# Performance work log

Hardware: AMD Instinct MI355X
Metric: run time of the kernel (lower is better)

## Reference

```python
import jax, jax.numpy as jnp
import numpy as np

C = 256
NUM_HEADS = 8
GROUPS = 8
EPS = 1e-5


def setup_inputs() -> dict:
    key = jax.random.key(0)
    ks = jax.random.split(key, 7)
    B, H, W = 2, 64, 64
    x = jax.random.normal(ks[0], (B, C, H, W), dtype=jnp.float32)
    gn_weight = jnp.ones((C,), dtype=jnp.float32)
    gn_bias = jnp.zeros((C,), dtype=jnp.float32)
    # 1x1 convs == per-pixel linear layers
    w_qkv = jax.random.normal(ks[1], (3 * C, C), dtype=jnp.float32) * (1.0 / np.sqrt(C))
    b_qkv = jax.random.normal(ks[2], (3 * C,), dtype=jnp.float32) * 0.01
    w_proj = jax.random.normal(ks[3], (C, C), dtype=jnp.float32) * (1.0 / np.sqrt(C))
    b_proj = jax.random.normal(ks[4], (C,), dtype=jnp.float32) * 0.01
    return {"x": x, "gn_weight": gn_weight, "gn_bias": gn_bias,
            "w_qkv": w_qkv, "b_qkv": b_qkv, "w_proj": w_proj, "b_proj": b_proj}


def reference(x, gn_weight, gn_bias, w_qkv, b_qkv, w_proj, b_proj):
    B, Cc, H, W = x.shape
    nh = NUM_HEADS
    hd = Cc // nh
    N = H * W
    scale = hd ** (-0.5)

    # GroupNorm(8, C): normalize over (C/G, H, W) per group, biased variance
    xg = x.reshape(B, GROUPS, Cc // GROUPS, H, W)
    mean = xg.mean(axis=(2, 3, 4), keepdims=True)
    var = xg.var(axis=(2, 3, 4), keepdims=True)
    hn = (xg - mean) * jax.lax.rsqrt(var + EPS)
    hn = hn.reshape(B, Cc, H, W) * gn_weight[None, :, None, None] + gn_bias[None, :, None, None]

    hf = hn.reshape(B, Cc, N)                       # [B, C, N]
    qkv = jnp.einsum('oc,bcn->bon', w_qkv, hf) + b_qkv[None, :, None]  # [B, 3C, N]
    qkv = qkv.reshape(B, 3, nh, hd, N)
    # q,k,v: [B, nh, N, hd]
    q = jnp.transpose(qkv[:, 0], (0, 1, 3, 2))
    k = jnp.transpose(qkv[:, 1], (0, 1, 3, 2))
    v = jnp.transpose(qkv[:, 2], (0, 1, 3, 2))

    attn = jnp.einsum('bhqd,bhkd->bhqk', q, k) * scale  # [B, nh, N, N]
    attn = jax.nn.softmax(attn, axis=-1)
    o = jnp.einsum('bhqk,bhkd->bhqd', attn, v)           # [B, nh, N, hd]
    o = jnp.transpose(o, (0, 1, 3, 2)).reshape(B, Cc, H, W)

    of = o.reshape(B, Cc, N)
    out = jnp.einsum('oc,bcn->bon', w_proj, of) + b_proj[None, :, None]
    return out.reshape(B, Cc, H, W)
```

## Files before the change

kernel.cpp:

```cpp
#include <hip/hip_runtime.h>


typedef _Float16 half8 __attribute__((ext_vector_type(8)));
typedef __fp16   fp16x2 __attribute__((ext_vector_type(2)));
typedef float    f32x4 __attribute__((ext_vector_type(4)));
typedef int      int2v __attribute__((ext_vector_type(2)));
typedef int      int4v __attribute__((ext_vector_type(4)));

__device__ __forceinline__ f32x4 mfma16(half8 a, half8 b, f32x4 c) {
  return __builtin_amdgcn_mfma_f32_16x16x32_f16(a, b, c, 0, 0, 0);
}

#if __has_builtin(__builtin_amdgcn_exp2f)
#define EXP2(x) __builtin_amdgcn_exp2f(x)
#else
#define EXP2(x) exp2f(x)
#endif

__device__ __forceinline__ unsigned short h_bits(_Float16 h) {
  return __builtin_bit_cast(unsigned short, h);
}
__device__ __forceinline__ int h2_bits(fp16x2 h) {
  return __builtin_bit_cast(int, h);
}

constexpr float CSCALE = (float)(1.4426950408889634 / 5.656854249492381);

__global__ __launch_bounds__(256) void gn_stats(const float* __restrict__ x,
                                                float* __restrict__ stats) {
  const int bg = blockIdx.x, ch = blockIdx.y, tid = threadIdx.x;
  const float* p = x + (size_t)bg * 131072 + (size_t)ch * 4096;
  float s = 0.f, ss = 0.f;
#pragma unroll
  for (int j = 0; j < 4; ++j) {
    f32x4 v = *(const f32x4*)(p + j * 1024 + tid * 4);
#pragma unroll
    for (int k = 0; k < 4; ++k) { s += v[k]; ss += v[k] * v[k]; }
  }
#pragma unroll
  for (int m = 1; m <= 32; m <<= 1) { s += __shfl_xor(s, m); ss += __shfl_xor(ss, m); }
  __shared__ float red[8];
  const int wv = tid >> 6;
  if ((tid & 63) == 0) { red[wv * 2] = s; red[wv * 2 + 1] = ss; }
  __syncthreads();
  if (tid == 0) {
    float S = red[0] + red[2] + red[4] + red[6];
    float SS = red[1] + red[3] + red[5] + red[7];
    atomicAdd(&stats[bg * 2], S);
    atomicAdd(&stats[bg * 2 + 1], SS);
  }
}

__global__ __launch_bounds__(256) void gn_apply(const float* __restrict__ x,
                                                const float* __restrict__ gw,
                                                const float* __restrict__ gb,
                                                const float* __restrict__ stats,
                                                _Float16* __restrict__ hn) {
  __shared__ float tile[64 * 65];
  const int tid = threadIdx.x;
  const int a = tid & 15;
  const int row16 = tid >> 4;
  const int b = blockIdx.z, c0 = blockIdx.y * 64, n0 = blockIdx.x * 64;
#pragma unroll
  for (int m = 0; m < 4; ++m) {
    const int cl = row16 + 16 * m;
    const int c = c0 + cl;
    const int g = c >> 5;
    const float s = stats[(b * 8 + g) * 2];
    const float ss = stats[(b * 8 + g) * 2 + 1];
    const float mean = s * (1.f / 131072.f);
    const float var = ss * (1.f / 131072.f) - mean * mean;
    const float rstd = rsqrtf(var + 1e-5f);
    const float ga = gw[c] * rstd;
    const float be = gb[c] - mean * ga;
    f32x4 xv = *(const f32x4*)(x + ((size_t)(b * 256 + c)) * 4096 + n0 + a * 4);
#pragma unroll
    for (int j = 0; j < 4; ++j) tile[cl * 65 + a * 4 + j] = xv[j] * ga + be;
  }
  __syncthreads();
#pragma unroll
  for (int m = 0; m < 4; ++m) {
    const int nl = row16 + 16 * m;
    const int cb = a * 4;
    int2v uh;
    unsigned short hh[4];
#pragma unroll
    for (int j = 0; j < 4; ++j) {
      hh[j] = h_bits((_Float16)tile[(cb + j) * 65 + nl]);
    }
    uh[0] = hh[0] | (hh[1] << 16); uh[1] = hh[2] | (hh[3] << 16);
    size_t off = ((size_t)(b * 4096 + n0 + nl)) * 256 + c0 + cb;
    *(int2v*)(hn + off) = uh;
  }
}

__global__ __launch_bounds__(256) void wcast(const float* __restrict__ wq,
                                             const float* __restrict__ wp,
                                             _Float16* __restrict__ wqh,
                                             _Float16* __restrict__ wph) {
  const int idx = blockIdx.x * 256 + threadIdx.x;
  if (idx < 196608) {
    wqh[idx] = (_Float16)wq[idx];
  } else {
    wph[idx - 196608] = (_Float16)wp[idx - 196608];
  }
}

template <int MODE>
__global__ __launch_bounds__(256) void gemm_f16(
    const _Float16* __restrict__ W, const _Float16* __restrict__ Bm,
    const float* __restrict__ bias,
    _Float16* __restrict__ qkT, _Float16* __restrict__ v_t,
    float* __restrict__ outp) {
  __shared__ _Float16 a_lds[2][4096];
  __shared__ _Float16 b_lds[2][4096];
  const int tid = threadIdx.x, lane = tid & 63, wv = tid >> 6;
  const int qq = lane >> 4, ii = lane & 15;
  const int m0 = blockIdx.x * 64, n0 = blockIdx.y * 64, bz = blockIdx.z;

  const _Float16* asrc[2];
  const _Float16* bsrc[2];
  int dst8[2];
#pragma unroll
  for (int rep = 0; rep < 2; ++rep) {
    const int idx = tid + 256 * rep;
    dst8[rep] = idx * 8;
    const int j = idx >> 7, c = (idx >> 6) & 1, l = idx & 63;
    const int lq = l >> 4, li = l & 15;
    asrc[rep] = W + (size_t)(m0 + 16 * j + li) * 256 + 32 * c + 8 * lq;
    bsrc[rep] = Bm + ((size_t)(bz * 4096 + n0 + 16 * j + li)) * 256 + 32 * c + 8 * lq;
  }

  f32x4 acc[4] = {};

  half8 ar0 = *(const half8*)asrc[0];
  half8 ar1 = *(const half8*)asrc[1];
  half8 br0 = *(const half8*)bsrc[0];
  half8 br1 = *(const half8*)bsrc[1];
  *(half8*)(a_lds[0] + dst8[0]) = ar0;
  *(half8*)(a_lds[0] + dst8[1]) = ar1;
  *(half8*)(b_lds[0] + dst8[0]) = br0;
  *(half8*)(b_lds[0] + dst8[1]) = br1;
  __syncthreads();

  for (int it = 0; it < 4; ++it) {
    const int cur = it & 1;
    if (it < 3) {
      const int ko = (it + 1) * 64;
      ar0 = *(const half8*)(asrc[0] + ko);
      ar1 = *(const half8*)(asrc[1] + ko);
      br0 = *(const half8*)(bsrc[0] + ko);
      br1 = *(const half8*)(bsrc[1] + ko);
    }
    half8 ah0 = *(const half8*)(a_lds[cur] + ((wv * 2 + 0) * 64 + lane) * 8);
    half8 ah1 = *(const half8*)(a_lds[cur] + ((wv * 2 + 1) * 64 + lane) * 8);
#pragma unroll
    for (int t = 0; t < 4; ++t) {
      half8 b0 = *(const half8*)(b_lds[cur] + ((t * 2 + 0) * 64 + lane) * 8);
      half8 b1 = *(const half8*)(b_lds[cur] + ((t * 2 + 1) * 64 + lane) * 8);
      acc[t] = mfma16(ah0, b0, acc[t]);
      acc[t] = mfma16(ah1, b1, acc[t]);
    }
    if (it < 3) {
      _Float16* an = a_lds[cur ^ 1];
      _Float16* bn = b_lds[cur ^ 1];
      *(half8*)(an + dst8[0]) = ar0;
      *(half8*)(an + dst8[1]) = ar1;
      *(half8*)(bn + dst8[0]) = br0;
      *(half8*)(bn + dst8[1]) = br1;
    }
    __syncthreads();
  }

  const int och0 = m0 + 16 * wv + 4 * qq;
  if (MODE == 0) {
    if (m0 < 512) {
      const float sc = (m0 < 256) ? CSCALE : 1.0f;
#pragma unroll
      for (int t = 0; t < 4; ++t) {
        const int n = n0 + 16 * t + ii;
        unsigned short hh[4];
#pragma unroll
        for (int r = 0; r < 4; ++r) {
          hh[r] = h_bits((_Float16)((acc[t][r] + bias[och0 + r]) * sc));
        }
        int2v u;
        u[0] = hh[0] | (hh[1] << 16);
        u[1] = hh[2] | (hh[3] << 16);
        *(int2v*)(qkT + ((size_t)(bz * 4096 + n)) * 512 + och0) = u;
      }
    } else {
#pragma unroll
      for (int t = 0; t < 4; ++t) {
#pragma unroll
        for (int r = 0; r < 4; ++r) {
          const int och = och0 + r;
          const int d = och - 512;
          const int hd_ = d & 31, head = d >> 5;
          const int n = n0 + 16 * t + ii;
          v_t[((size_t)((bz * 8 + head) * 32 + hd_)) * 4096 + n] =
              (_Float16)(acc[t][r] + bias[och]);
        }
      }
    }
  } else {
#pragma unroll
    for (int t = 0; t < 4; ++t) {
#pragma unroll
      for (int r = 0; r < 4; ++r) {
        const int och = och0 + r;
        const int n = n0 + 16 * t + ii;
        outp[((size_t)(bz * 256 + och)) * 4096 + n] = acc[t][r] + bias[och];
      }
    }
  }
}

__global__ __launch_bounds__(256) void attn_kernel(
    const _Float16* __restrict__ qkT, const _Float16* __restrict__ v_t,
    float* __restrict__ opart, float* __restrict__ lpart, int nkb) {
  __shared__ _Float16 k_lds[2][2048];
  __shared__ _Float16 v_lds[2][2048];
  const int tid = threadIdx.x, lane = tid & 63, wv = tid >> 6;
  const int qq = lane >> 4, ii = lane & 15;
  const int bh = blockIdx.y, b = bh >> 3, h = bh & 7;
  const int n0 = blockIdx.x * 128;
  const int part = blockIdx.z;
  const int key0 = part * (nkb * 64);

  const _Float16* qbase =
      qkT + ((size_t)(b * 4096 + n0 + 32 * wv + ii)) * 512 + h * 32 + 8 * qq;
  half8 qf0 = *(const half8*)qbase;
  half8 qf1 = *(const half8*)(qbase + (size_t)16 * 512);

  const int dst8 = tid * 8;
  const int f = tid >> 6, l = tid & 63;
  const int fq = l >> 4, fi = l & 15;
  const int su = f >> 1, shf = f & 1;
  const int g = 32 * su + 4 * shf + 8 * (fi >> 2) + (fi & 3);
  const _Float16* ksrc =
      qkT + ((size_t)(b * 4096 + key0 + g)) * 512 + 256 + h * 32 + 8 * fq;
  const _Float16* vsrc =
      v_t + ((size_t)(bh * 32 + 16 * shf + fi)) * 4096 + key0 + 32 * su + 8 * fq;

  half8 ones8;
#pragma unroll
  for (int j = 0; j < 8; ++j) ones8[j] = (_Float16)1.0f;

  f32x4 o00 = {}, o10 = {}, o01 = {}, o11 = {}, accl0 = {}, accl1 = {};

  half8 kr = *(const half8*)ksrc;
  half8 vr = *(const half8*)vsrc;
  *(half8*)(k_lds[0] + dst8) = kr;
  *(half8*)(v_lds[0] + dst8) = vr;
  __syncthreads();

  for (int kb = 0; kb < nkb; ++kb) {
    const int cur = kb & 1;
    if (kb < nkb - 1) {
      kr = *(const half8*)(ksrc + (size_t)(kb + 1) * (64 * 512));
      vr = *(const half8*)(vsrc + (size_t)(kb + 1) * 64);
    }
    const _Float16* kbase = k_lds[cur];
    const _Float16* vbase = v_lds[cur];

#pragma unroll
    for (int u = 0; u < 2; ++u) {
      half8 kfa = *(const half8*)(kbase + u * 1024 + lane * 8);
      half8 kfb = *(const half8*)(kbase + u * 1024 + 512 + lane * 8);
      f32x4 z = {};
      f32x4 sa0 = mfma16(kfa, qf0, z);
      f32x4 sb0 = mfma16(kfb, qf0, z);
      f32x4 sa1 = mfma16(kfa, qf1, z);
      f32x4 sb1 = mfma16(kfb, qf1, z);
      int4v p0, p1;
      p0[0] = h2_bits(__builtin_amdgcn_cvt_pkrtz(EXP2(sa0[0]), EXP2(sa0[1])));
      p0[1] = h2_bits(__builtin_amdgcn_cvt_pkrtz(EXP2(sa0[2]), EXP2(sa0[3])));
      p0[2] = h2_bits(__builtin_amdgcn_cvt_pkrtz(EXP2(sb0[0]), EXP2(sb0[1])));
      p0[3] = h2_bits(__builtin_amdgcn_cvt_pkrtz(EXP2(sb0[2]), EXP2(sb0[3])));
      p1[0] = h2_bits(__builtin_amdgcn_cvt_pkrtz(EXP2(sa1[0]), EXP2(sa1[1])));
      p1[1] = h2_bits(__builtin_amdgcn_cvt_pkrtz(EXP2(sa1[2]), EXP2(sa1[3])));
      p1[2] = h2_bits(__builtin_amdgcn_cvt_pkrtz(EXP2(sb1[0]), EXP2(sb1[1])));
      p1[3] = h2_bits(__builtin_amdgcn_cvt_pkrtz(EXP2(sb1[2]), EXP2(sb1[3])));
      half8 pt0 = __builtin_bit_cast(half8, p0);
      half8 pt1 = __builtin_bit_cast(half8, p1);
      half8 vf0 = *(const half8*)(vbase + u * 1024 + lane * 8);
      half8 vf1 = *(const half8*)(vbase + u * 1024 + 512 + lane * 8);
      o00 = mfma16(vf0, pt0, o00);
      o10 = mfma16(vf1, pt0, o10);
      accl0 = mfma16(ones8, pt0, accl0);
      o01 = mfma16(vf0, pt1, o01);
      o11 = mfma16(vf1, pt1, o11);
      accl1 = mfma16(ones8, pt1, accl1);
    }

    if (kb < nkb - 1) {
      *(half8*)(k_lds[cur ^ 1] + dst8) = kr;
      *(half8*)(v_lds[cur ^ 1] + dst8) = vr;
    }
    __syncthreads();
  }

#pragma unroll
  for (int hf = 0; hf < 2; ++hf) {
    const f32x4 oa = hf ? o01 : o00;
    const f32x4 ob = hf ? o11 : o10;
    const int q = n0 + 32 * wv + 16 * hf + ii;
    float* base = opart + ((size_t)((part * 2 + b) * 4096 + q)) * 256 + h * 32;
    *(f32x4*)(base + 4 * qq) = oa;
    *(f32x4*)(base + 16 + 4 * qq) = ob;
    if (qq == 0) {
      lpart[((size_t)((part * 2 + b) * 4096 + q)) * 8 + h] = hf ? accl1[0] : accl0[0];
    }
  }
}

__global__ __launch_bounds__(256) void attn_combine(
    const float* __restrict__ opart, const float* __restrict__ lpart,
    _Float16* __restrict__ o16, int parts) {
  const int c = threadIdx.x, hh = c >> 5;
#pragma unroll
  for (int k = 0; k < 4; ++k) {
    const int row = blockIdx.x * 4 + k;
    const int b = row >> 12;
    const int q = row & 4095;
    float O = 0.f, L = 0.f;
    for (int p = 0; p < parts; ++p) {
      O += opart[((size_t)((p * 2 + b) * 4096 + q)) * 256 + c];
      L += lpart[((size_t)((p * 2 + b) * 4096 + q)) * 8 + hh];
    }
    const float inv = 1.0f / L;
    o16[(size_t)row * 256 + c] = (_Float16)(O * inv);
  }
}

extern "C" void kernel_launch(void* const* d_in, const int* in_sizes, int n_in,
                              void* d_out, int out_size, void* d_ws, size_t ws_size,
                              hipStream_t stream) {
  const float* x     = (const float*)d_in[0];
  const float* gnw   = (const float*)d_in[1];
  const float* gnb   = (const float*)d_in[2];
  const float* wqkv  = (const float*)d_in[3];
  const float* bqkv  = (const float*)d_in[4];
  const float* wproj = (const float*)d_in[5];
  const float* bproj = (const float*)d_in[6];
  float* out = (float*)d_out;

  char* ws = (char*)d_ws;
  size_t off = 0;
  auto alloc = [&](size_t bytes) -> char* {
    char* p = ws + off;
    off += (bytes + 255) & ~(size_t)255;
    return p;
  };
  float*    stats  = (float*)alloc(128);
  _Float16* hn     = (_Float16*)alloc((size_t)2 * 4096 * 256 * 2);
  _Float16* wq_h   = (_Float16*)alloc((size_t)768 * 256 * 2);
  _Float16* wp_h   = (_Float16*)alloc((size_t)256 * 256 * 2);
  _Float16* qkT    = (_Float16*)alloc((size_t)2 * 4096 * 512 * 2);
  _Float16* v_t    = (_Float16*)alloc((size_t)16 * 32 * 4096 * 2);

  int parts = 4;
  {
    const size_t need4 = (size_t)8 * 4096 * 256 * 4 + (size_t)8 * 4096 * 8 * 4 + 1024;
    if (off + need4 > ws_size) parts = 2;
  }
  float*    opart  = (float*)alloc((size_t)(parts * 2) * 4096 * 256 * 4);
  float*    lpart  = (float*)alloc((size_t)(parts * 2) * 4096 * 8 * 4);
  _Float16* o16 = hn;
  if (off > ws_size) return;

  (void)hipMemsetAsync(stats, 0, 256, stream);
  gn_stats<<<dim3(16, 32), 256, 0, stream>>>(x, stats);
  gn_apply<<<dim3(64, 4, 2), 256, 0, stream>>>(x, gnw, gnb, stats, hn);
  wcast<<<1024, 256, 0, stream>>>(wqkv, wproj, wq_h, wp_h);
  gemm_f16<0><<<dim3(12, 64, 2), 256, 0, stream>>>(wq_h, hn, bqkv, qkT, v_t,
                                                   nullptr);
  const int nkb = 64 / parts;
  attn_kernel<<<dim3(32, 16, parts), 256, 0, stream>>>(qkT, v_t, opart, lpart,
                                                       nkb);
  attn_combine<<<2048, 256, 0, stream>>>(opart, lpart, o16, parts);
  gemm_f16<1><<<dim3(4, 64, 2), 256, 0, stream>>>(wp_h, o16, bproj, nullptr,
                                                  nullptr, out);
}
```

Baseline: 168.0 us.

## Use direct global-to-LDS loads with 4-stage K/V ring in attention

Replaces the register-staged double buffer for K/V tiles with global_load_lds direct-to-LDS copies into a four-slot ring, prefetching two tiles ahead. Synchronisation changes to vmcnt waits plus a raw s_barrier, and the trailing __syncthreads is removed. The combine kernel is also vectorised to four floats per thread with packed fp16 stores. This aims to hide global load latency and remove the VGPR round trip. The cost is twice the LDS footprint, and removing the end-of-iteration barrier is only safe because the ring is deep enough that no slot is overwritten while still being read.

```diff
diff --git a/kernel.cpp b/kernel.cpp
--- a/kernel.cpp
+++ b/kernel.cpp
@@ -22,6 +22,12 @@
 }
 __device__ __forceinline__ int h2_bits(fp16x2 h) {
   return __builtin_bit_cast(int, h);
+}
+
+__device__ __forceinline__ void gl16(const _Float16* g, _Float16* l) {
+  __builtin_amdgcn_global_load_lds(
+      (const __attribute__((address_space(1))) unsigned int*)g,
+      (__attribute__((address_space(3))) unsigned int*)l, 16, 0, 0);
 }
 
 constexpr float CSCALE = (float)(1.4426950408889634 / 5.656854249492381);
@@ -219,8 +225,8 @@
 __global__ __launch_bounds__(256) void attn_kernel(
     const _Float16* __restrict__ qkT, const _Float16* __restrict__ v_t,
     float* __restrict__ opart, float* __restrict__ lpart, int nkb) {
-  __shared__ _Float16 k_lds[2][2048];
-  __shared__ _Float16 v_lds[2][2048];
+  __shared__ _Float16 k_lds[4][2048];
+  __shared__ _Float16 v_lds[4][2048];
   const int tid = threadIdx.x, lane = tid & 63, wv = tid >> 6;
   const int qq = lane >> 4, ii = lane & 15;
   const int bh = blockIdx.y, b = bh >> 3, h = bh & 7;
@@ -233,7 +239,6 @@
   half8 qf0 = *(const half8*)qbase;
   half8 qf1 = *(const half8*)(qbase + (size_t)16 * 512);
 
-  const int dst8 = tid * 8;
   const int f = tid >> 6, l = tid & 63;
   const int fq = l >> 4, fi = l & 15;
   const int su = f >> 1, shf = f & 1;
@@ -242,6 +247,7 @@
       qkT + ((size_t)(b * 4096 + key0 + g)) * 512 + 256 + h * 32 + 8 * fq;
   const _Float16* vsrc =
       v_t + ((size_t)(bh * 32 + 16 * shf + fi)) * 4096 + key0 + 32 * su + 8 * fq;
+  const int wb = wv * 512;
 
   half8 ones8;
 #pragma unroll
@@ -249,21 +255,30 @@
 
   f32x4 o00 = {}, o10 = {}, o01 = {}, o11 = {}, accl0 = {}, accl1 = {};
 
-  half8 kr = *(const half8*)ksrc;
-  half8 vr = *(const half8*)vsrc;
-  *(half8*)(k_lds[0] + dst8) = kr;
-  *(half8*)(v_lds[0] + dst8) = vr;
-  __syncthreads();
-
+  gl16(ksrc, &k_lds[0][wb]);
+  gl16(vsrc, &v_lds[0][wb]);
+  gl16(ksrc + 32768, &k_lds[1][wb]);
+  gl16(vsrc + 64, &v_lds[1][wb]);
+
+  int cur = 0;
   for (int kb = 0; kb < nkb; ++kb) {
-    const int cur = kb & 1;
-    if (kb < nkb - 1) {
-      kr = *(const half8*)(ksrc + (size_t)(kb + 1) * (64 * 512));
-      vr = *(const half8*)(vsrc + (size_t)(kb + 1) * 64);
-    }
+    if (kb + 2 < nkb) {
+      const int pb = (cur + 2) & 3;
+      gl16(ksrc + (size_t)(kb + 2) * 32768, &k_lds[pb][wb]);
+      gl16(vsrc + (size_t)(kb + 2) * 64, &v_lds[pb][wb]);
+    }
+    if (kb < nkb - 2) {
+      asm volatile("s_waitcnt vmcnt(4)" ::: "memory");
+    } else if (kb == nkb - 2) {
+      asm volatile("s_waitcnt vmcnt(2)" ::: "memory");
+    } else {
+      asm volatile("s_waitcnt vmcnt(0)" ::: "memory");
+    }
+    __builtin_amdgcn_s_barrier();
+    __builtin_amdgcn_sched_barrier(0);
+
     const _Float16* kbase = k_lds[cur];
     const _Float16* vbase = v_lds[cur];
-
 #pragma unroll
     for (int u = 0; u < 2; ++u) {
       half8 kfa = *(const half8*)(kbase + u * 1024 + lane * 8);
@@ -293,12 +308,7 @@
       o11 = mfma16(vf1, pt1, o11);
       accl1 = mfma16(ones8, pt1, accl1);
     }
-
-    if (kb < nkb - 1) {
-      *(half8*)(k_lds[cur ^ 1] + dst8) = kr;
-      *(half8*)(v_lds[cur ^ 1] + dst8) = vr;
-    }
-    __syncthreads();
+    cur = (cur + 1) & 3;
   }
 
 #pragma unroll
@@ -318,20 +328,28 @@
 __global__ __launch_bounds__(256) void attn_combine(
     const float* __restrict__ opart, const float* __restrict__ lpart,
     _Float16* __restrict__ o16, int parts) {
-  const int c = threadIdx.x, hh = c >> 5;
-#pragma unroll
-  for (int k = 0; k < 4; ++k) {
-    const int row = blockIdx.x * 4 + k;
-    const int b = row >> 12;
-    const int q = row & 4095;
-    float O = 0.f, L = 0.f;
-    for (int p = 0; p < parts; ++p) {
-      O += opart[((size_t)((p * 2 + b) * 4096 + q)) * 256 + c];
-      L += lpart[((size_t)((p * 2 + b) * 4096 + q)) * 8 + hh];
-    }
-    const float inv = 1.0f / L;
-    o16[(size_t)row * 256 + c] = (_Float16)(O * inv);
-  }
+  const int t = threadIdx.x;
+  const int cq = (t & 63) * 4;
+  const int kr = t >> 6;
+  const int row = blockIdx.x * 4 + kr;
+  const int b = row >> 12;
+  const int q = row & 4095;
+  const int hh = cq >> 5;
+  f32x4 O = {};
+  float L = 0.f;
+  for (int p = 0; p < parts; ++p) {
+    const size_t rbase = ((size_t)((p * 2 + b) * 4096 + q));
+    O += *(const f32x4*)(opart + rbase * 256 + cq);
+    L += lpart[rbase * 8 + hh];
+  }
+  const float inv = 1.0f / L;
+  unsigned short hw[4];
+#pragma unroll
+  for (int j = 0; j < 4; ++j) hw[j] = h_bits((_Float16)(O[j] * inv));
+  int2v u;
+  u[0] = hw[0] | (hw[1] << 16);
+  u[1] = hw[2] | (hw[3] << 16);
+  *(int2v*)(o16 + (size_t)row * 256 + cq) = u;
 }
 
 extern "C" void kernel_launch(void* const* d_in, const int* in_sizes, int n_in,
```

Measured after the change: 169.2 us. About the same (+0.7%).
